# Performance work log

Measured on AMD Instinct MI355X. Metric: run time of the kernel, lower is better.

Reference implementation:

```python
import jax, jax.numpy as jnp
import numpy as np

B, T, C, MULT, ND, H = 32, 512, 384, 4, 16, 1024
D = C * MULT            # input_dim = 1536
SIZE, STRIDE = 4, 2     # stack kernel / stride
L = (T - SIZE) // STRIDE + 1  # 255 stacked frames
MAXF = 512
SCALE = float(H) ** 0.5  # config.scale == None -> sqrt(hidden_size)


def setup_inputs() -> dict:
    key = jax.random.key(0)
    ks = jax.random.split(key, 8)
    return {
        "spikes": jax.random.normal(ks[0], (B, T, C), jnp.float32),
        "spikes_mask": jax.random.randint(ks[1], (B, T), 0, 2).astype(jnp.int32),
        "spikes_timestamp": jax.random.randint(ks[2], (B, T), 0, MAXF),
        "date_idx": jax.random.randint(ks[3], (B,), 0, ND),
        "W_embed": jax.random.normal(ks[4], (ND, D, C), jnp.float32) * 0.02,
        "b_embed": jnp.zeros((ND, D), jnp.float32),
        "W_proj": jax.random.normal(ks[5], (H, SIZE * D), jnp.float32) * 0.02,
        "b_proj": jnp.zeros((H,), jnp.float32),
        "pos_table": jax.random.normal(ks[6], (MAXF, H), jnp.float32) * 0.02,
    }


def reference(spikes, spikes_mask, spikes_timestamp, date_idx,
              W_embed, b_embed, W_proj, b_proj, pos_table):
    # --- adaptive per-date linear: grouped GEMM instead of per-sample loop ---
    Wg = W_embed[date_idx]          # [B, D, C]
    bg = b_embed[date_idx]          # [B, D]
    x = jnp.einsum('btc,bdc->btd', spikes, Wg) + bg[:, None, :]  # [B, T, D]
    # act * scale (torch 'gelu' is exact erf gelu)
    x = jax.nn.gelu(x, approximate=False) * SCALE
    # --- unfold-stack: windows of SIZE frames, stride STRIDE ---
    starts = jnp.arange(L) * STRIDE
    win = starts[:, None] + jnp.arange(SIZE)          # [L, SIZE]
    patches = x[:, win, :].reshape(B, L, SIZE * D)    # [B, L, SIZE*D] (kh-major = torch unfold order)
    x = patches @ W_proj.T + b_proj                   # [B, L, H]
    # stacked mask: product of window mask entries
    mask = jnp.prod(spikes_mask[:, win], axis=-1).astype(spikes_mask.dtype)  # [B, L]
    ts = spikes_timestamp[:, :L]                      # [B, L]
    # positional embedding add; dropout p=0 -> identity
    x = x + pos_table[ts]
    return x, mask, ts
```

## Files before the change

### kernel.cpp

```cpp
#include <hip/hip_runtime.h>
#include <hip/hip_bf16.h>

#define B_    32
#define T_    512
#define C_    384
#define D_    1536
#define H_    1024
#define L_    255
#define KP_   6144
#define ND_   16

#define BUFB 49152

using f32x4 = __attribute__((ext_vector_type(4))) float;
using s16x8 = __attribute__((ext_vector_type(8))) short;
using i32x4 = __attribute__((ext_vector_type(4))) int;
using i32x8 = __attribute__((ext_vector_type(8))) int;

__device__ __forceinline__ void gld_lds16(const void* g, void* l) {
    __builtin_amdgcn_global_load_lds(
        (const __attribute__((address_space(1))) void*)g,
        (__attribute__((address_space(3))) void*)l,
        16, 0, 0);
}

__device__ __forceinline__ f32x4 MFMA(s16x8 a, s16x8 b, f32x4 c) {
    return __builtin_amdgcn_mfma_f32_16x16x32_bf16(a, b, c, 0, 0, 0);
}

__device__ __forceinline__ f32x4 MFMA8(i32x8 a, i32x8 b, f32x4 c) {
    return __builtin_amdgcn_mfma_scale_f32_16x16x128_f8f6f4(
        a, b, c, 0, 0, 0, 0x7F7F7F7F, 0, 0x7B7B7B7B);
}

__global__ __launch_bounds__(256) void prep(
    const float* __restrict__ sp, const float* __restrict__ we,
    const float* __restrict__ wp, const int* __restrict__ mIn,
    const int* __restrict__ tIn,
    __hip_bfloat16* __restrict__ spB, __hip_bfloat16* __restrict__ weB,
    unsigned char* __restrict__ wp8, float* __restrict__ out) {
    int id = blockIdx.x * 256 + threadIdx.x;
    if (id < 3932160) {
        const float* src; __hip_bfloat16* dst; int idx;
        if (id < 1572864) { src = sp; dst = spB; idx = id; }
        else              { src = we; dst = weB; idx = id - 1572864; }
        float4 v = reinterpret_cast<const float4*>(src)[idx];
        __hip_bfloat16 o[4] = {__float2bfloat16(v.x), __float2bfloat16(v.y),
                               __float2bfloat16(v.z), __float2bfloat16(v.w)};
        reinterpret_cast<ushort4*>(dst)[idx] = *reinterpret_cast<ushort4*>(o);
    } else if (id < 5505024) {
        int idx = id - 3932160;
        float4 v = reinterpret_cast<const float4*>(wp)[idx];
        int w = __builtin_amdgcn_cvt_pk_fp8_f32(v.x * 16.f, v.y * 16.f, 0, false);
        w = __builtin_amdgcn_cvt_pk_fp8_f32(v.z * 16.f, v.w * 16.f, w, true);
        reinterpret_cast<int*>(wp8)[idx] = w;
    } else {
        int i = id - 5505024;
        if (i < B_ * L_) {
            int b = i / L_, l = i % L_;
            const int* mb = mIn + b * T_ + 2 * l;
            int m = mb[0] * mb[1] * mb[2] * mb[3];
            const size_t offM = (size_t)B_ * L_ * H_;
            out[offM + i] = (float)m;
            out[offM + (size_t)B_ * L_ + i] = (float)tIn[b * T_ + l];
        }
    }
}

__device__ __forceinline__ void tile_compute(const char* la, const char* lb,
                                             f32x4 (&acc)[4][4],
                                             int rA, int rB, int g) {
    const int sxA = rA & 7, sxB = rB & 7;
    s16x8 af0[4], bf0[4], af1[4], bf1[4];
    #pragma unroll
    for (int mi = 0; mi < 4; ++mi)
        af0[mi] = *(const s16x8*)(la + rA * 128 + mi * 2048 + ((g ^ sxA) << 4));
    #pragma unroll
    for (int ni = 0; ni < 4; ++ni)
        bf0[ni] = *(const s16x8*)(lb + rB * 128 + ni * 2048 + ((g ^ sxB) << 4));
    #pragma unroll
    for (int mi = 0; mi < 4; ++mi)
        af1[mi] = *(const s16x8*)(la + rA * 128 + mi * 2048 + (((4 + g) ^ sxA) << 4));
    #pragma unroll
    for (int ni = 0; ni < 4; ++ni)
        bf1[ni] = *(const s16x8*)(lb + rB * 128 + ni * 2048 + (((4 + g) ^ sxB) << 4));
    asm volatile("s_waitcnt lgkmcnt(8)" ::: "memory");
    __builtin_amdgcn_sched_barrier(0);
    __builtin_amdgcn_s_setprio(1);
    #pragma unroll
    for (int mi = 0; mi < 4; ++mi)
        #pragma unroll
        for (int ni = 0; ni < 4; ++ni)
            acc[mi][ni] = MFMA(af0[mi], bf0[ni], acc[mi][ni]);
    __builtin_amdgcn_s_setprio(0);
    asm volatile("s_waitcnt lgkmcnt(0)" ::: "memory");
    __builtin_amdgcn_sched_barrier(0);
    __builtin_amdgcn_s_setprio(1);
    #pragma unroll
    for (int mi = 0; mi < 4; ++mi)
        #pragma unroll
        for (int ni = 0; ni < 4; ++ni)
            acc[mi][ni] = MFMA(af1[mi], bf1[ni], acc[mi][ni]);
    __builtin_amdgcn_s_setprio(0);
}

__global__ __launch_bounds__(512, 2) void gemm1_embed(
    const __hip_bfloat16* __restrict__ Sp,
    const __hip_bfloat16* __restrict__ We,
    const float* __restrict__ bEmb,
    const int* __restrict__ dateIdx,
    unsigned char* __restrict__ X18) {
    extern __shared__ __align__(16) char lds[];
    const int tid  = threadIdx.x;
    const int lane = tid & 63, wid = tid >> 6;
    const int wr = wid >> 1, wc = wid & 1;
    const int id   = blockIdx.x;
    const int xcd  = id & 7, slot = id >> 3;
    const int b    = xcd * 4 + slot / 24;
    const int tile = slot % 24;
    const int m0   = (tile % 2) * 256;
    const int n0   = (tile / 2) * 128;
    const int didx = dateIdx[b];
    const __hip_bfloat16* A  = Sp + (size_t)b * T_ * C_;
    const __hip_bfloat16* Bm = We + (size_t)didx * D_ * C_;
    const int KT = C_ / 64;

    auto stage = [&](int kt, int buf) {
        char* lA = lds + buf * BUFB;
        char* lB = lA + 32768;
        int k0 = kt * 64;
        #pragma unroll
        for (int i = 0; i < 4; ++i) {
            int p = i * 512 + tid;
            int row = p >> 3;
            int clog = (p & 7) ^ (row & 7);
            gld_lds16(A + (size_t)(m0 + row) * C_ + k0 + clog * 8,
                      lA + (i * 512 + wid * 64) * 16);
        }
        #pragma unroll
        for (int i = 0; i < 2; ++i) {
            int p = i * 512 + tid;
            int row = p >> 3;
            int clog = (p & 7) ^ (row & 7);
            gld_lds16(Bm + (size_t)(n0 + row) * C_ + k0 + clog * 8,
                      lB + (i * 512 + wid * 64) * 16);
        }
    };

    f32x4 acc[4][4] = {};
    const int rl = lane & 15, g = lane >> 4;
    const int rA = wr * 64 + rl, rB = wc * 64 + rl;

    stage(0, 0);
    stage(1, 1);
    for (int kt = 0; kt < KT - 2; ++kt) {
        stage(kt + 2, (kt + 2) % 3);
        asm volatile("s_waitcnt vmcnt(12)" ::: "memory");
        __builtin_amdgcn_s_barrier();
        const char* la = lds + (kt % 3) * BUFB;
        tile_compute(la, la + 32768, acc, rA, rB, g);
        __builtin_amdgcn_s_barrier();
    }
    asm volatile("s_waitcnt vmcnt(6)" ::: "memory");
    __builtin_amdgcn_s_barrier();
    {
        const char* la = lds + ((KT - 2) % 3) * BUFB;
        tile_compute(la, la + 32768, acc, rA, rB, g);
    }
    asm volatile("s_waitcnt vmcnt(0)" ::: "memory");
    __builtin_amdgcn_s_barrier();
    {
        const char* la = lds + ((KT - 1) % 3) * BUFB;
        tile_compute(la, la + 32768, acc, rA, rB, g);
    }

    #pragma unroll
    for (int mi = 0; mi < 4; ++mi) {
        #pragma unroll
        for (int ni = 0; ni < 4; ++ni) {
            int col = n0 + wc * 64 + ni * 16 + rl;
            float bg = bEmb[didx * D_ + col];
            #pragma unroll
            for (int r = 0; r < 4; ++r) {
                int row = m0 + wr * 64 + mi * 16 + g * 4 + r;
                float v = acc[mi][ni][r] + bg;
                float gl = 0.5f * v * (1.0f + erff(v * 0.70710678118f)) * 32.0f;
                int pk = __builtin_amdgcn_cvt_pk_fp8_f32(gl, gl, 0, false);
                X18[((size_t)b * T_ + row) * D_ + col] = (unsigned char)pk;
            }
        }
    }
}

__global__ __launch_bounds__(512, 4) void gemm2_proj(
    const unsigned char* __restrict__ X18,
    const unsigned char* __restrict__ Wp8,
    const float* __restrict__ bProj,
    const float* __restrict__ posTab,
    const int* __restrict__ tsIn,
    float* __restrict__ outX) {
    extern __shared__ __align__(16) char lds2[];
    const int tid  = threadIdx.x;
    const int lane = tid & 63, wid = tid >> 6;
    const int wm = wid >> 2, wn = wid & 3;
    const int id   = blockIdx.x;
    const int xcd  = id & 7, slot = id >> 3;
    const int b    = xcd * 4 + (slot >> 4);
    const int t    = slot & 15;
    const int m0   = (t & 1) * 128;
    const int n0   = (t >> 1) * 128;
    const unsigned char* Xb = X18 + (size_t)b * T_ * D_;
    const int KT = 48;

    const unsigned char* aP[2]; const unsigned char* bP[2]; int dstC[2];
    #pragma unroll
    for (int i = 0; i < 2; ++i) {
        int p = i * 512 + tid;
        int row = p >> 3;
        int c = (p & 7) ^ (row & 7);
        int l = m0 + row; if (l > 254) l = 254;
        aP[i] = Xb + (size_t)(2 * l) * D_ + c * 16;
        bP[i] = Wp8 + (size_t)(n0 + row) * KP_ + c * 16;
        dstC[i] = (i * 512 + wid * 64) * 16;
    }
    auto stage = [&](int kt, int buf) {
        int ko = (kt & 3) * D_ + (kt >> 2) * 128;
        char* base = lds2 + buf * 32768;
        #pragma unroll
        for (int i = 0; i < 2; ++i) {
            gld_lds16(aP[i] + ko, base + dstC[i]);
            gld_lds16(bP[i] + ko, base + 16384 + dstC[i]);
        }
    };

    const int rl = lane & 15, g = lane >> 4, sx = rl & 7;
    const int ck0 = ((2 * g) ^ sx) << 4;
    const int ck1 = ((2 * g + 1) ^ sx) << 4;
    int aOff[4], bOff[2];
    #pragma unroll
    for (int mi = 0; mi < 4; ++mi) aOff[mi] = (wm * 64 + mi * 16 + rl) * 128;
    #pragma unroll
    for (int ni = 0; ni < 2; ++ni) bOff[ni] = 16384 + (wn * 32 + ni * 16 + rl) * 128;

    union u8x32 { i32x8 v; i32x4 h[2]; };
    f32x4 acc[4][2] = {};

    stage(0, 0);
    for (int u = 0; u < KT; ++u) {
        int buf = u & 1;
        char* base = lds2 + buf * 32768;
        if (u + 1 < KT) {
            stage(u + 1, buf ^ 1);
            asm volatile("s_waitcnt vmcnt(4)" ::: "memory");
        } else {
            asm volatile("s_waitcnt vmcnt(0)" ::: "memory");
        }
        __builtin_amdgcn_s_barrier();

        u8x32 A[4], Bv[2];
        #pragma unroll
        for (int mi = 0; mi < 4; ++mi) {
            A[mi].h[0] = *(const i32x4*)(base + aOff[mi] + ck0);
            A[mi].h[1] = *(const i32x4*)(base + aOff[mi] + ck1);
        }
        #pragma unroll
        for (int ni = 0; ni < 2; ++ni) {
            Bv[ni].h[0] = *(const i32x4*)(base + bOff[ni] + ck0);
            Bv[ni].h[1] = *(const i32x4*)(base + bOff[ni] + ck1);
        }
        #pragma unroll
        for (int ni = 0; ni < 2; ++ni)
            #pragma unroll
            for (int mi = 0; mi < 4; ++mi)
                acc[mi][ni] = MFMA8(A[mi].v, Bv[ni].v, acc[mi][ni]);
        __builtin_amdgcn_s_barrier();
    }

    #pragma unroll
    for (int mi = 0; mi < 4; ++mi) {
        #pragma unroll
        for (int ni = 0; ni < 2; ++ni) {
            int h = n0 + wn * 32 + ni * 16 + rl;
            float bp = bProj[h];
            #pragma unroll
            for (int r = 0; r < 4; ++r) {
                int l = m0 + wm * 64 + mi * 16 + g * 4 + r;
                if (l < L_) {
                    int tsv = tsIn[b * T_ + l];
                    float v = acc[mi][ni][r] + bp + posTab[(size_t)tsv * H_ + h];
                    outX[((size_t)b * L_ + l) * H_ + h] = v;
                }
            }
        }
    }
}

extern "C" void kernel_launch(void* const* d_in, const int* in_sizes, int n_in,
                              void* d_out, int out_size, void* d_ws, size_t ws_size,
                              hipStream_t stream) {
    (void)in_sizes; (void)n_in; (void)out_size; (void)ws_size;
    const float* spikes  = (const float*)d_in[0];
    const int*   smask   = (const int*)d_in[1];
    const int*   sts     = (const int*)d_in[2];
    const int*   dateIdx = (const int*)d_in[3];
    const float* Wemb    = (const float*)d_in[4];
    const float* bEmb    = (const float*)d_in[5];
    const float* Wproj   = (const float*)d_in[6];
    const float* bProj   = (const float*)d_in[7];
    const float* posTab  = (const float*)d_in[8];
    float* out = (float*)d_out;

    char* ws = (char*)d_ws;
    unsigned char*  X18 = (unsigned char*)(ws);
    __hip_bfloat16* SpB = (__hip_bfloat16*)(ws + 25165824);
    __hip_bfloat16* WeB = (__hip_bfloat16*)(ws + 37748736);
    unsigned char*  Wp8 = (unsigned char*)(ws + 56623104);

    hipFuncSetAttribute((const void*)gemm1_embed,
                        hipFuncAttributeMaxDynamicSharedMemorySize, 3 * BUFB);
    hipFuncSetAttribute((const void*)gemm2_proj,
                        hipFuncAttributeMaxDynamicSharedMemorySize, 65536);

    prep<<<21536, 256, 0, stream>>>(spikes, Wemb, Wproj, smask, sts,
                                    SpB, WeB, Wp8, out);

    gemm1_embed<<<768, 512, 3 * BUFB, stream>>>(SpB, WeB, bEmb, dateIdx, X18);

    gemm2_proj<<<512, 512, 65536, stream>>>(X18, Wp8, bProj, posTab, sts, out);
}
```

Baseline: 124.1 us.

## Load gemm2 A operand directly from global into registers, stage only B in LDS

In the projection GEMM, each wave now reads its A fragments (the fp8 GELU activations) straight from global memory into registers instead of staging them through LDS. Only the weight tile B is double-buffered in static LDS, which halves LDS use and drops the dynamic shared-memory allocation. The wait counts are retuned for the new load mix, and the MFMA block is wrapped in sched_barrier and setprio. Waves in the same column now load the same A rows redundantly from global or L2, and the global loads may not be coalesced as well as the staged path was.

```diff
diff --git a/kernel.cpp b/kernel.cpp
--- a/kernel.cpp
+++ b/kernel.cpp
@@ -199,7 +199,7 @@
     const float* __restrict__ posTab,
     const int* __restrict__ tsIn,
     float* __restrict__ outX) {
-    extern __shared__ __align__(16) char lds2[];
+    __shared__ __align__(16) char ldsB[2][16384];
     const int tid  = threadIdx.x;
     const int lane = tid & 63, wid = tid >> 6;
     const int wm = wid >> 2, wn = wid & 3;
@@ -212,67 +212,79 @@
     const unsigned char* Xb = X18 + (size_t)b * T_ * D_;
     const int KT = 48;
 
-    const unsigned char* aP[2]; const unsigned char* bP[2]; int dstC[2];
-    #pragma unroll
-    for (int i = 0; i < 2; ++i) {
-        int p = i * 512 + tid;
-        int row = p >> 3;
-        int c = (p & 7) ^ (row & 7);
-        int l = m0 + row; if (l > 254) l = 254;
-        aP[i] = Xb + (size_t)(2 * l) * D_ + c * 16;
-        bP[i] = Wp8 + (size_t)(n0 + row) * KP_ + c * 16;
-        dstC[i] = (i * 512 + wid * 64) * 16;
-    }
-    auto stage = [&](int kt, int buf) {
-        int ko = (kt & 3) * D_ + (kt >> 2) * 128;
-        char* base = lds2 + buf * 32768;
-        #pragma unroll
-        for (int i = 0; i < 2; ++i) {
-            gld_lds16(aP[i] + ko, base + dstC[i]);
-            gld_lds16(bP[i] + ko, base + 16384 + dstC[i]);
-        }
-    };
+    const unsigned char* bP0; const unsigned char* bP1;
+    int dstC0, dstC1;
+    {
+        int p = tid, row = p >> 3, c = (p & 7) ^ (row & 7);
+        bP0 = Wp8 + (size_t)(n0 + row) * KP_ + c * 16;
+        dstC0 = (wid * 64) * 16;
+        p = 512 + tid; row = p >> 3; c = (p & 7) ^ (row & 7);
+        bP1 = Wp8 + (size_t)(n0 + row) * KP_ + c * 16;
+        dstC1 = (512 + wid * 64) * 16;
+    }
 
     const int rl = lane & 15, g = lane >> 4, sx = rl & 7;
+    const unsigned char* aA0; const unsigned char* aA1;
+    const unsigned char* aA2; const unsigned char* aA3;
+    {
+        int l0 = m0 + wm * 64 + rl;
+        int l1 = l0 + 16, l2 = l0 + 32, l3 = l0 + 48;
+        if (l0 > 254) l0 = 254; if (l1 > 254) l1 = 254;
+        if (l2 > 254) l2 = 254; if (l3 > 254) l3 = 254;
+        aA0 = Xb + (size_t)(2 * l0) * D_ + g * 32;
+        aA1 = Xb + (size_t)(2 * l1) * D_ + g * 32;
+        aA2 = Xb + (size_t)(2 * l2) * D_ + g * 32;
+        aA3 = Xb + (size_t)(2 * l3) * D_ + g * 32;
+    }
+
     const int ck0 = ((2 * g) ^ sx) << 4;
     const int ck1 = ((2 * g + 1) ^ sx) << 4;
-    int aOff[4], bOff[2];
-    #pragma unroll
-    for (int mi = 0; mi < 4; ++mi) aOff[mi] = (wm * 64 + mi * 16 + rl) * 128;
-    #pragma unroll
-    for (int ni = 0; ni < 2; ++ni) bOff[ni] = 16384 + (wn * 32 + ni * 16 + rl) * 128;
-
-    union u8x32 { i32x8 v; i32x4 h[2]; };
+    const int bOff0 = (wn * 32 + rl) * 128;
+    const int bOff1 = (wn * 32 + 16 + rl) * 128;
+
+    union U8 { i32x8 v; i32x4 h[2]; };
     f32x4 acc[4][2] = {};
 
-    stage(0, 0);
+    gld_lds16(bP0, &ldsB[0][dstC0]);
+    gld_lds16(bP1, &ldsB[0][dstC1]);
+
     for (int u = 0; u < KT; ++u) {
         int buf = u & 1;
-        char* base = lds2 + buf * 32768;
+        int ko = u * 128;
+        U8 A0, A1, A2, A3;
+        A0.h[0] = *(const i32x4*)(aA0 + ko); A0.h[1] = *(const i32x4*)(aA0 + ko + 16);
+        A1.h[0] = *(const i32x4*)(aA1 + ko); A1.h[1] = *(const i32x4*)(aA1 + ko + 16);
+        A2.h[0] = *(const i32x4*)(aA2 + ko); A2.h[1] = *(const i32x4*)(aA2 + ko + 16);
+        A3.h[0] = *(const i32x4*)(aA3 + ko); A3.h[1] = *(const i32x4*)(aA3 + ko + 16);
+        __builtin_amdgcn_sched_barrier(0);
         if (u + 1 < KT) {
-            stage(u + 1, buf ^ 1);
-            asm volatile("s_waitcnt vmcnt(4)" ::: "memory");
+            gld_lds16(bP0 + ko + 128, &ldsB[buf ^ 1][dstC0]);
+            gld_lds16(bP1 + ko + 128, &ldsB[buf ^ 1][dstC1]);
+            __builtin_amdgcn_sched_barrier(0);
+            asm volatile("s_waitcnt vmcnt(10)" ::: "memory");
         } else {
-            asm volatile("s_waitcnt vmcnt(0)" ::: "memory");
+            asm volatile("s_waitcnt vmcnt(8)" ::: "memory");
         }
         __builtin_amdgcn_s_barrier();
 
-        u8x32 A[4], Bv[2];
-        #pragma unroll
-        for (int mi = 0; mi < 4; ++mi) {
-            A[mi].h[0] = *(const i32x4*)(base + aOff[mi] + ck0);
-            A[mi].h[1] = *(const i32x4*)(base + aOff[mi] + ck1);
-        }
-        #pragma unroll
-        for (int ni = 0; ni < 2; ++ni) {
-            Bv[ni].h[0] = *(const i32x4*)(base + bOff[ni] + ck0);
-            Bv[ni].h[1] = *(const i32x4*)(base + bOff[ni] + ck1);
-        }
-        #pragma unroll
-        for (int ni = 0; ni < 2; ++ni)
-            #pragma unroll
-            for (int mi = 0; mi < 4; ++mi)
-                acc[mi][ni] = MFMA8(A[mi].v, Bv[ni].v, acc[mi][ni]);
+        U8 Bv0, Bv1;
+        Bv0.h[0] = *(const i32x4*)(&ldsB[buf][0] + bOff0 + ck0);
+        Bv0.h[1] = *(const i32x4*)(&ldsB[buf][0] + bOff0 + ck1);
+        Bv1.h[0] = *(const i32x4*)(&ldsB[buf][0] + bOff1 + ck0);
+        Bv1.h[1] = *(const i32x4*)(&ldsB[buf][0] + bOff1 + ck1);
+        if (u + 1 < KT) { asm volatile("s_waitcnt vmcnt(2) lgkmcnt(0)" ::: "memory"); }
+        else            { asm volatile("s_waitcnt vmcnt(0) lgkmcnt(0)" ::: "memory"); }
+        __builtin_amdgcn_sched_barrier(0);
+        __builtin_amdgcn_s_setprio(1);
+        acc[0][0] = MFMA8(A0.v, Bv0.v, acc[0][0]);
+        acc[1][0] = MFMA8(A1.v, Bv0.v, acc[1][0]);
+        acc[2][0] = MFMA8(A2.v, Bv0.v, acc[2][0]);
+        acc[3][0] = MFMA8(A3.v, Bv0.v, acc[3][0]);
+        acc[0][1] = MFMA8(A0.v, Bv1.v, acc[0][1]);
+        acc[1][1] = MFMA8(A1.v, Bv1.v, acc[1][1]);
+        acc[2][1] = MFMA8(A2.v, Bv1.v, acc[2][1]);
+        acc[3][1] = MFMA8(A3.v, Bv1.v, acc[3][1]);
+        __builtin_amdgcn_s_setprio(0);
         __builtin_amdgcn_s_barrier();
     }
 
@@ -318,13 +330,11 @@
 
     hipFuncSetAttribute((const void*)gemm1_embed,
                         hipFuncAttributeMaxDynamicSharedMemorySize, 3 * BUFB);
-    hipFuncSetAttribute((const void*)gemm2_proj,
-                        hipFuncAttributeMaxDynamicSharedMemorySize, 65536);
 
     prep<<<21536, 256, 0, stream>>>(spikes, Wemb, Wproj, smask, sts,
                                     SpB, WeB, Wp8, out);
 
     gemm1_embed<<<768, 512, 3 * BUFB, stream>>>(SpB, WeB, bEmb, dateIdx, X18);
 
-    gemm2_proj<<<512, 512, 65536, stream>>>(X18, Wp8, bProj, posTab, sts, out);
-}
+    gemm2_proj<<<512, 512, 0, stream>>>(X18, Wp8, bProj, posTab, sts, out);
+}
```

Measured after the change: 264.3 us. 2.13x slower.

## Restructure projection GEMM to 32x32x64 FP8 MFMA with 128x256 tiles and triple buffering

Applied to the files above, without the earlier changes.

The projection GEMM now uses the 32x32x64 scaled FP8 MFMA instead of 16x16x128. Each block computes a 128x256 output tile with a K step of 64, so there are 256 blocks instead of 512. The double-buffered LDS pipeline becomes a three-stage ring with a new swizzle, and LDS reads are interleaved with MFMAs using waitcnt, sched_barrier and setprio. The goal is fewer LDS reads per FLOP and better latency hiding. The cost is more K iterations with a barrier pair each, and half as many blocks, which may leave CUs underfilled.

```diff
diff --git a/kernel.cpp b/kernel.cpp
--- a/kernel.cpp
+++ b/kernel.cpp
@@ -11,11 +11,13 @@
 #define ND_   16
 
 #define BUFB 49152
-
-using f32x4 = __attribute__((ext_vector_type(4))) float;
-using s16x8 = __attribute__((ext_vector_type(8))) short;
-using i32x4 = __attribute__((ext_vector_type(4))) int;
-using i32x8 = __attribute__((ext_vector_type(8))) int;
+#define G2BUF 24576
+
+using f32x4  = __attribute__((ext_vector_type(4))) float;
+using f32x16 = __attribute__((ext_vector_type(16))) float;
+using s16x8  = __attribute__((ext_vector_type(8))) short;
+using i32x4  = __attribute__((ext_vector_type(4))) int;
+using i32x8  = __attribute__((ext_vector_type(8))) int;
 
 __device__ __forceinline__ void gld_lds16(const void* g, void* l) {
     __builtin_amdgcn_global_load_lds(
@@ -28,8 +30,8 @@
     return __builtin_amdgcn_mfma_f32_16x16x32_bf16(a, b, c, 0, 0, 0);
 }
 
-__device__ __forceinline__ f32x4 MFMA8(i32x8 a, i32x8 b, f32x4 c) {
-    return __builtin_amdgcn_mfma_scale_f32_16x16x128_f8f6f4(
+__device__ __forceinline__ f32x16 MFMA8W(i32x8 a, i32x8 b, f32x16 c) {
+    return __builtin_amdgcn_mfma_scale_f32_32x32x64_f8f6f4(
         a, b, c, 0, 0, 0, 0x7F7F7F7F, 0, 0x7B7B7B7B);
 }
 
@@ -192,7 +194,7 @@
     }
 }
 
-__global__ __launch_bounds__(512, 4) void gemm2_proj(
+__global__ __launch_bounds__(512, 2) void gemm2_proj(
     const unsigned char* __restrict__ X18,
     const unsigned char* __restrict__ Wp8,
     const float* __restrict__ bProj,
@@ -205,86 +207,107 @@
     const int wm = wid >> 2, wn = wid & 3;
     const int id   = blockIdx.x;
     const int xcd  = id & 7, slot = id >> 3;
-    const int b    = xcd * 4 + (slot >> 4);
-    const int t    = slot & 15;
+    const int b    = xcd * 4 + (slot >> 3);
+    const int t    = slot & 7;
     const int m0   = (t & 1) * 128;
-    const int n0   = (t >> 1) * 128;
+    const int n0   = (t >> 1) * 256;
     const unsigned char* Xb = X18 + (size_t)b * T_ * D_;
-    const int KT = 48;
-
-    const unsigned char* aP[2]; const unsigned char* bP[2]; int dstC[2];
-    #pragma unroll
-    for (int i = 0; i < 2; ++i) {
-        int p = i * 512 + tid;
-        int row = p >> 3;
-        int c = (p & 7) ^ (row & 7);
+    const int KT = 96;
+
+    const unsigned char* aSrc;
+    {
+        int row = tid >> 2;
+        int cl = (tid & 3) ^ ((row >> 2) & 3);
         int l = m0 + row; if (l > 254) l = 254;
-        aP[i] = Xb + (size_t)(2 * l) * D_ + c * 16;
-        bP[i] = Wp8 + (size_t)(n0 + row) * KP_ + c * 16;
-        dstC[i] = (i * 512 + wid * 64) * 16;
+        aSrc = Xb + (size_t)(2 * l) * D_ + cl * 16;
+    }
+    const unsigned char* bSrc0; const unsigned char* bSrc1;
+    {
+        int p = tid, row = p >> 2, cl = (p & 3) ^ ((row >> 2) & 3);
+        bSrc0 = Wp8 + (size_t)(n0 + row) * KP_ + cl * 16;
+        p = 512 + tid; row = p >> 2; cl = (p & 3) ^ ((row >> 2) & 3);
+        bSrc1 = Wp8 + (size_t)(n0 + row) * KP_ + cl * 16;
     }
     auto stage = [&](int kt, int buf) {
-        int ko = (kt & 3) * D_ + (kt >> 2) * 128;
-        char* base = lds2 + buf * 32768;
-        #pragma unroll
-        for (int i = 0; i < 2; ++i) {
-            gld_lds16(aP[i] + ko, base + dstC[i]);
-            gld_lds16(bP[i] + ko, base + 16384 + dstC[i]);
-        }
+        int ko = kt * 64;
+        char* base = lds2 + buf * G2BUF;
+        gld_lds16(aSrc + ko, base + tid * 16);
+        gld_lds16(bSrc0 + ko, base + 8192 + tid * 16);
+        gld_lds16(bSrc1 + ko, base + 8192 + (512 + tid) * 16);
     };
 
-    const int rl = lane & 15, g = lane >> 4, sx = rl & 7;
-    const int ck0 = ((2 * g) ^ sx) << 4;
-    const int ck1 = ((2 * g + 1) ^ sx) << 4;
-    int aOff[4], bOff[2];
-    #pragma unroll
-    for (int mi = 0; mi < 4; ++mi) aOff[mi] = (wm * 64 + mi * 16 + rl) * 128;
-    #pragma unroll
-    for (int ni = 0; ni < 2; ++ni) bOff[ni] = 16384 + (wn * 32 + ni * 16 + rl) * 128;
-
-    union u8x32 { i32x8 v; i32x4 h[2]; };
-    f32x4 acc[4][2] = {};
+    const int l31 = lane & 31, kg = lane >> 5;
+    int aOff[2][2], bOff[2][2];
+    #pragma unroll
+    for (int mi = 0; mi < 2; ++mi) {
+        int row = wm * 64 + mi * 32 + l31;
+        int sw = (row >> 2) & 3;
+        aOff[mi][0] = row * 64 + (((kg * 2) ^ sw) << 4);
+        aOff[mi][1] = row * 64 + (((kg * 2 + 1) ^ sw) << 4);
+    }
+    #pragma unroll
+    for (int ni = 0; ni < 2; ++ni) {
+        int row = wn * 64 + ni * 32 + l31;
+        int sw = (row >> 2) & 3;
+        bOff[ni][0] = 8192 + row * 64 + (((kg * 2) ^ sw) << 4);
+        bOff[ni][1] = 8192 + row * 64 + (((kg * 2 + 1) ^ sw) << 4);
+    }
+
+    union U8 { i32x8 v; i32x4 h[2]; };
+    f32x16 acc[2][2] = {};
 
     stage(0, 0);
+    stage(1, 1);
     for (int u = 0; u < KT; ++u) {
-        int buf = u & 1;
-        char* base = lds2 + buf * 32768;
-        if (u + 1 < KT) {
-            stage(u + 1, buf ^ 1);
-            asm volatile("s_waitcnt vmcnt(4)" ::: "memory");
+        if (u + 2 < KT) {
+            stage(u + 2, (u + 2) % 3);
+            asm volatile("s_waitcnt vmcnt(6)" ::: "memory");
+        } else if (u + 1 < KT) {
+            asm volatile("s_waitcnt vmcnt(3)" ::: "memory");
         } else {
             asm volatile("s_waitcnt vmcnt(0)" ::: "memory");
         }
         __builtin_amdgcn_s_barrier();
 
-        u8x32 A[4], Bv[2];
-        #pragma unroll
-        for (int mi = 0; mi < 4; ++mi) {
-            A[mi].h[0] = *(const i32x4*)(base + aOff[mi] + ck0);
-            A[mi].h[1] = *(const i32x4*)(base + aOff[mi] + ck1);
-        }
+        const char* base = lds2 + (u % 3) * G2BUF;
+        U8 A0, A1, B0, B1;
+        A0.h[0] = *(const i32x4*)(base + aOff[0][0]);
+        A0.h[1] = *(const i32x4*)(base + aOff[0][1]);
+        B0.h[0] = *(const i32x4*)(base + bOff[0][0]);
+        B0.h[1] = *(const i32x4*)(base + bOff[0][1]);
+        A1.h[0] = *(const i32x4*)(base + aOff[1][0]);
+        A1.h[1] = *(const i32x4*)(base + aOff[1][1]);
+        B1.h[0] = *(const i32x4*)(base + bOff[1][0]);
+        B1.h[1] = *(const i32x4*)(base + bOff[1][1]);
+        asm volatile("s_waitcnt lgkmcnt(4)" ::: "memory");
+        __builtin_amdgcn_sched_barrier(0);
+        __builtin_amdgcn_s_setprio(1);
+        acc[0][0] = MFMA8W(A0.v, B0.v, acc[0][0]);
+        __builtin_amdgcn_s_setprio(0);
+        asm volatile("s_waitcnt lgkmcnt(2)" ::: "memory");
+        __builtin_amdgcn_sched_barrier(0);
+        __builtin_amdgcn_s_setprio(1);
+        acc[1][0] = MFMA8W(A1.v, B0.v, acc[1][0]);
+        __builtin_amdgcn_s_setprio(0);
+        asm volatile("s_waitcnt lgkmcnt(0)" ::: "memory");
+        __builtin_amdgcn_sched_barrier(0);
+        __builtin_amdgcn_s_setprio(1);
+        acc[0][1] = MFMA8W(A0.v, B1.v, acc[0][1]);
+        acc[1][1] = MFMA8W(A1.v, B1.v, acc[1][1]);
+        __builtin_amdgcn_s_setprio(0);
+        __builtin_amdgcn_s_barrier();
+    }
+
+    #pragma unroll
+    for (int mi = 0; mi < 2; ++mi) {
         #pragma unroll
         for (int ni = 0; ni < 2; ++ni) {
-            Bv[ni].h[0] = *(const i32x4*)(base + bOff[ni] + ck0);
-            Bv[ni].h[1] = *(const i32x4*)(base + bOff[ni] + ck1);
-        }
-        #pragma unroll
-        for (int ni = 0; ni < 2; ++ni)
-            #pragma unroll
-            for (int mi = 0; mi < 4; ++mi)
-                acc[mi][ni] = MFMA8(A[mi].v, Bv[ni].v, acc[mi][ni]);
-        __builtin_amdgcn_s_barrier();
-    }
-
-    #pragma unroll
-    for (int mi = 0; mi < 4; ++mi) {
-        #pragma unroll
-        for (int ni = 0; ni < 2; ++ni) {
-            int h = n0 + wn * 32 + ni * 16 + rl;
+            int h = n0 + wn * 64 + ni * 32 + l31;
             float bp = bProj[h];
             #pragma unroll
-            for (int r = 0; r < 4; ++r) {
-                int l = m0 + wm * 64 + mi * 16 + g * 4 + r;
+            for (int r = 0; r < 16; ++r) {
+                int row = (r & 3) + 8 * (r >> 2) + 4 * kg;
+                int l = m0 + wm * 64 + mi * 32 + row;
                 if (l < L_) {
                     int tsv = tsIn[b * T_ + l];
                     float v = acc[mi][ni][r] + bp + posTab[(size_t)tsv * H_ + h];
@@ -319,12 +342,12 @@
     hipFuncSetAttribute((const void*)gemm1_embed,
                         hipFuncAttributeMaxDynamicSharedMemorySize, 3 * BUFB);
     hipFuncSetAttribute((const void*)gemm2_proj,
-                        hipFuncAttributeMaxDynamicSharedMemorySize, 65536);
+                        hipFuncAttributeMaxDynamicSharedMemorySize, 3 * G2BUF);
 
     prep<<<21536, 256, 0, stream>>>(spikes, Wemb, Wproj, smask, sts,
                                     SpB, WeB, Wp8, out);
 
     gemm1_embed<<<768, 512, 3 * BUFB, stream>>>(SpB, WeB, bEmb, dateIdx, X18);
 
-    gemm2_proj<<<512, 512, 65536, stream>>>(X18, Wp8, bProj, posTab, sts, out);
-}
+    gemm2_proj<<<256, 512, 3 * G2BUF, stream>>>(X18, Wp8, bProj, posTab, sts, out);
+}
```

After: 142.8 us. 15.1% more time.

## Switch embed GEMM to FP8 scaled MFMA with smaller tiles and double buffering

Applied to the files above, without the earlier changes.

The spikes and embedding weights are now quantized to FP8 in the prep kernel instead of BF16, with a scale of 16 on the weights. The first GEMM uses the 16x16x128 scaled FP8 MFMA with K=128 steps, so only 3 iterations are needed. Tiles shrink to 128x128 with double-buffered 64KB LDS, the grid doubles to 1536 blocks, and occupancy rises to 4 blocks per CU. This cuts conversion write and read traffic and MFMA issue count, but quantizing the raw normal spikes to FP8 lowers accuracy.

```diff
diff --git a/kernel.cpp b/kernel.cpp
--- a/kernel.cpp
+++ b/kernel.cpp
@@ -10,10 +10,8 @@
 #define KP_   6144
 #define ND_   16
 
-#define BUFB 49152
 
 using f32x4 = __attribute__((ext_vector_type(4))) float;
-using s16x8 = __attribute__((ext_vector_type(8))) short;
 using i32x4 = __attribute__((ext_vector_type(4))) int;
 using i32x8 = __attribute__((ext_vector_type(8))) int;
 
@@ -24,10 +22,6 @@
         16, 0, 0);
 }
 
-__device__ __forceinline__ f32x4 MFMA(s16x8 a, s16x8 b, f32x4 c) {
-    return __builtin_amdgcn_mfma_f32_16x16x32_bf16(a, b, c, 0, 0, 0);
-}
-
 __device__ __forceinline__ f32x4 MFMA8(i32x8 a, i32x8 b, f32x4 c) {
     return __builtin_amdgcn_mfma_scale_f32_16x16x128_f8f6f4(
         a, b, c, 0, 0, 0, 0x7F7F7F7F, 0, 0x7B7B7B7B);
@@ -37,23 +31,18 @@
     const float* __restrict__ sp, const float* __restrict__ we,
     const float* __restrict__ wp, const int* __restrict__ mIn,
     const int* __restrict__ tIn,
-    __hip_bfloat16* __restrict__ spB, __hip_bfloat16* __restrict__ weB,
+    unsigned char* __restrict__ sp8, unsigned char* __restrict__ we8,
     unsigned char* __restrict__ wp8, float* __restrict__ out) {
     int id = blockIdx.x * 256 + threadIdx.x;
-    if (id < 3932160) {
-        const float* src; __hip_bfloat16* dst; int idx;
-        if (id < 1572864) { src = sp; dst = spB; idx = id; }
-        else              { src = we; dst = weB; idx = id - 1572864; }
+    if (id < 5505024) {
+        const float* src; unsigned char* dst; int idx; float s;
+        if (id < 1572864)      { src = sp; dst = sp8; idx = id;           s = 1.f;  }
+        else if (id < 3932160) { src = we; dst = we8; idx = id - 1572864; s = 16.f; }
+        else                   { src = wp; dst = wp8; idx = id - 3932160; s = 16.f; }
         float4 v = reinterpret_cast<const float4*>(src)[idx];
-        __hip_bfloat16 o[4] = {__float2bfloat16(v.x), __float2bfloat16(v.y),
-                               __float2bfloat16(v.z), __float2bfloat16(v.w)};
-        reinterpret_cast<ushort4*>(dst)[idx] = *reinterpret_cast<ushort4*>(o);
-    } else if (id < 5505024) {
-        int idx = id - 3932160;
-        float4 v = reinterpret_cast<const float4*>(wp)[idx];
-        int w = __builtin_amdgcn_cvt_pk_fp8_f32(v.x * 16.f, v.y * 16.f, 0, false);
-        w = __builtin_amdgcn_cvt_pk_fp8_f32(v.z * 16.f, v.w * 16.f, w, true);
-        reinterpret_cast<int*>(wp8)[idx] = w;
+        int w = __builtin_amdgcn_cvt_pk_fp8_f32(v.x * s, v.y * s, 0, false);
+        w = __builtin_amdgcn_cvt_pk_fp8_f32(v.z * s, v.w * s, w, true);
+        reinterpret_cast<int*>(dst)[idx] = w;
     } else {
         int i = id - 5505024;
         if (i < B_ * L_) {
@@ -67,122 +56,99 @@
     }
 }
 
-__device__ __forceinline__ void tile_compute(const char* la, const char* lb,
-                                             f32x4 (&acc)[4][4],
-                                             int rA, int rB, int g) {
-    const int sxA = rA & 7, sxB = rB & 7;
-    s16x8 af0[4], bf0[4], af1[4], bf1[4];
-    #pragma unroll
-    for (int mi = 0; mi < 4; ++mi)
-        af0[mi] = *(const s16x8*)(la + rA * 128 + mi * 2048 + ((g ^ sxA) << 4));
-    #pragma unroll
-    for (int ni = 0; ni < 4; ++ni)
-        bf0[ni] = *(const s16x8*)(lb + rB * 128 + ni * 2048 + ((g ^ sxB) << 4));
-    #pragma unroll
-    for (int mi = 0; mi < 4; ++mi)
-        af1[mi] = *(const s16x8*)(la + rA * 128 + mi * 2048 + (((4 + g) ^ sxA) << 4));
-    #pragma unroll
-    for (int ni = 0; ni < 4; ++ni)
-        bf1[ni] = *(const s16x8*)(lb + rB * 128 + ni * 2048 + (((4 + g) ^ sxB) << 4));
-    asm volatile("s_waitcnt lgkmcnt(8)" ::: "memory");
-    __builtin_amdgcn_sched_barrier(0);
-    __builtin_amdgcn_s_setprio(1);
-    #pragma unroll
-    for (int mi = 0; mi < 4; ++mi)
-        #pragma unroll
-        for (int ni = 0; ni < 4; ++ni)
-            acc[mi][ni] = MFMA(af0[mi], bf0[ni], acc[mi][ni]);
-    __builtin_amdgcn_s_setprio(0);
-    asm volatile("s_waitcnt lgkmcnt(0)" ::: "memory");
-    __builtin_amdgcn_sched_barrier(0);
-    __builtin_amdgcn_s_setprio(1);
-    #pragma unroll
-    for (int mi = 0; mi < 4; ++mi)
-        #pragma unroll
-        for (int ni = 0; ni < 4; ++ni)
-            acc[mi][ni] = MFMA(af1[mi], bf1[ni], acc[mi][ni]);
-    __builtin_amdgcn_s_setprio(0);
-}
-
-__global__ __launch_bounds__(512, 2) void gemm1_embed(
-    const __hip_bfloat16* __restrict__ Sp,
-    const __hip_bfloat16* __restrict__ We,
+__global__ __launch_bounds__(512, 4) void gemm1_embed(
+    const unsigned char* __restrict__ Sp8,
+    const unsigned char* __restrict__ We8,
     const float* __restrict__ bEmb,
     const int* __restrict__ dateIdx,
     unsigned char* __restrict__ X18) {
-    extern __shared__ __align__(16) char lds[];
+    extern __shared__ __align__(16) char lds1[];
     const int tid  = threadIdx.x;
     const int lane = tid & 63, wid = tid >> 6;
-    const int wr = wid >> 1, wc = wid & 1;
+    const int wm = wid >> 2, wn = wid & 3;
     const int id   = blockIdx.x;
     const int xcd  = id & 7, slot = id >> 3;
-    const int b    = xcd * 4 + slot / 24;
-    const int tile = slot % 24;
-    const int m0   = (tile % 2) * 256;
-    const int n0   = (tile / 2) * 128;
+    const int b    = xcd * 4 + slot / 48;
+    const int tile = slot % 48;
+    const int m0   = (tile & 3) * 128;
+    const int n0   = (tile >> 2) * 128;
     const int didx = dateIdx[b];
-    const __hip_bfloat16* A  = Sp + (size_t)b * T_ * C_;
-    const __hip_bfloat16* Bm = We + (size_t)didx * D_ * C_;
-    const int KT = C_ / 64;
-
+    const unsigned char* A  = Sp8 + (size_t)b * T_ * C_;
+    const unsigned char* Bm = We8 + (size_t)didx * D_ * C_;
+    const int KT = 3;
+
+    const unsigned char* aP[2]; const unsigned char* bP[2]; int dstC[2];
+    #pragma unroll
+    for (int i = 0; i < 2; ++i) {
+        int p = i * 512 + tid;
+        int row = p >> 3;
+        int c = (p & 7) ^ (row & 7);
+        aP[i] = A + (size_t)(m0 + row) * C_ + c * 16;
+        bP[i] = Bm + (size_t)(n0 + row) * C_ + c * 16;
+        dstC[i] = (i * 512 + wid * 64) * 16;
+    }
     auto stage = [&](int kt, int buf) {
-        char* lA = lds + buf * BUFB;
-        char* lB = lA + 32768;
-        int k0 = kt * 64;
-        #pragma unroll
-        for (int i = 0; i < 4; ++i) {
-            int p = i * 512 + tid;
-            int row = p >> 3;
-            int clog = (p & 7) ^ (row & 7);
-            gld_lds16(A + (size_t)(m0 + row) * C_ + k0 + clog * 8,
-                      lA + (i * 512 + wid * 64) * 16);
-        }
+        int ko = kt * 128;
+        char* base = lds1 + buf * 32768;
         #pragma unroll
         for (int i = 0; i < 2; ++i) {
-            int p = i * 512 + tid;
-            int row = p >> 3;
-            int clog = (p & 7) ^ (row & 7);
-            gld_lds16(Bm + (size_t)(n0 + row) * C_ + k0 + clog * 8,
-                      lB + (i * 512 + wid * 64) * 16);
+            gld_lds16(aP[i] + ko, base + dstC[i]);
+            gld_lds16(bP[i] + ko, base + 16384 + dstC[i]);
         }
     };
 
-    f32x4 acc[4][4] = {};
-    const int rl = lane & 15, g = lane >> 4;
-    const int rA = wr * 64 + rl, rB = wc * 64 + rl;
+    const int rl = lane & 15, g = lane >> 4, sx = rl & 7;
+    const int ck0 = ((2 * g) ^ sx) << 4;
+    const int ck1 = ((2 * g + 1) ^ sx) << 4;
+    int aOff[4], bOff[2];
+    #pragma unroll
+    for (int mi = 0; mi < 4; ++mi) aOff[mi] = (wm * 64 + mi * 16 + rl) * 128;
+    #pragma unroll
+    for (int ni = 0; ni < 2; ++ni) bOff[ni] = 16384 + (wn * 32 + ni * 16 + rl) * 128;
+
+    union u8x32 { i32x8 v; i32x4 h[2]; };
+    f32x4 acc[4][2] = {};
 
     stage(0, 0);
-    stage(1, 1);
-    for (int kt = 0; kt < KT - 2; ++kt) {
-        stage(kt + 2, (kt + 2) % 3);
-        asm volatile("s_waitcnt vmcnt(12)" ::: "memory");
-        __builtin_amdgcn_s_barrier();
-        const char* la = lds + (kt % 3) * BUFB;
-        tile_compute(la, la + 32768, acc, rA, rB, g);
-        __builtin_amdgcn_s_barrier();
-    }
-    asm volatile("s_waitcnt vmcnt(6)" ::: "memory");
-    __builtin_amdgcn_s_barrier();
-    {
-        const char* la = lds + ((KT - 2) % 3) * BUFB;
-        tile_compute(la, la + 32768, acc, rA, rB, g);
-    }
-    asm volatile("s_waitcnt vmcnt(0)" ::: "memory");
-    __builtin_amdgcn_s_barrier();
-    {
-        const char* la = lds + ((KT - 1) % 3) * BUFB;
-        tile_compute(la, la + 32768, acc, rA, rB, g);
+    for (int u = 0; u < KT; ++u) {
+        int buf = u & 1;
+        char* base = lds1 + buf * 32768;
+        if (u + 1 < KT) {
+            stage(u + 1, buf ^ 1);
+            asm volatile("s_waitcnt vmcnt(4)" ::: "memory");
+        } else {
+            asm volatile("s_waitcnt vmcnt(0)" ::: "memory");
+        }
+        __builtin_amdgcn_s_barrier();
+
+        u8x32 Af[4], Bv[2];
+        #pragma unroll
+        for (int mi = 0; mi < 4; ++mi) {
+            Af[mi].h[0] = *(const i32x4*)(base + aOff[mi] + ck0);
+            Af[mi].h[1] = *(const i32x4*)(base + aOff[mi] + ck1);
+        }
+        #pragma unroll
+        for (int ni = 0; ni < 2; ++ni) {
+            Bv[ni].h[0] = *(const i32x4*)(base + bOff[ni] + ck0);
+            Bv[ni].h[1] = *(const i32x4*)(base + bOff[ni] + ck1);
+        }
+        #pragma unroll
+        for (int ni = 0; ni < 2; ++ni)
+            #pragma unroll
+            for (int mi = 0; mi < 4; ++mi)
+                acc[mi][ni] = MFMA8(Af[mi].v, Bv[ni].v, acc[mi][ni]);
+        __builtin_amdgcn_s_barrier();
     }
 
     #pragma unroll
     for (int mi = 0; mi < 4; ++mi) {
         #pragma unroll
-        for (int ni = 0; ni < 4; ++ni) {
-            int col = n0 + wc * 64 + ni * 16 + rl;
+        for (int ni = 0; ni < 2; ++ni) {
+            int col = n0 + wn * 32 + ni * 16 + rl;
             float bg = bEmb[didx * D_ + col];
             #pragma unroll
             for (int r = 0; r < 4; ++r) {
-                int row = m0 + wr * 64 + mi * 16 + g * 4 + r;
+                int row = m0 + wm * 64 + mi * 16 + g * 4 + r;
                 float v = acc[mi][ni][r] + bg;
                 float gl = 0.5f * v * (1.0f + erff(v * 0.70710678118f)) * 32.0f;
                 int pk = __builtin_amdgcn_cvt_pk_fp8_f32(gl, gl, 0, false);
@@ -311,20 +277,20 @@
     float* out = (float*)d_out;
 
     char* ws = (char*)d_ws;
-    unsigned char*  X18 = (unsigned char*)(ws);
-    __hip_bfloat16* SpB = (__hip_bfloat16*)(ws + 25165824);
-    __hip_bfloat16* WeB = (__hip_bfloat16*)(ws + 37748736);
-    unsigned char*  Wp8 = (unsigned char*)(ws + 56623104);
+    unsigned char* X18 = (unsigned char*)(ws);
+    unsigned char* Sp8 = (unsigned char*)(ws + 25165824);
+    unsigned char* We8 = (unsigned char*)(ws + 31457280);
+    unsigned char* Wp8 = (unsigned char*)(ws + 40894464);
 
     hipFuncSetAttribute((const void*)gemm1_embed,
-                        hipFuncAttributeMaxDynamicSharedMemorySize, 3 * BUFB);
+                        hipFuncAttributeMaxDynamicSharedMemorySize, 65536);
     hipFuncSetAttribute((const void*)gemm2_proj,
                         hipFuncAttributeMaxDynamicSharedMemorySize, 65536);
 
     prep<<<21536, 256, 0, stream>>>(spikes, Wemb, Wproj, smask, sts,
-                                    SpB, WeB, Wp8, out);
-
-    gemm1_embed<<<768, 512, 3 * BUFB, stream>>>(SpB, WeB, bEmb, dateIdx, X18);
+                                    Sp8, We8, Wp8, out);
+
+    gemm1_embed<<<1536, 512, 65536, stream>>>(Sp8, We8, bEmb, dateIdx, X18);
 
     gemm2_proj<<<512, 512, 65536, stream>>>(X18, Wp8, bProj, posTab, sts, out);
 }
```

Result: slower. 141.3 us (+13.8%).
